# Kernel tuning notes

Measured on AMD Instinct MI355X. Metric: run time of the kernel, lower is better.

## Reference

```python
import jax, jax.numpy as jnp
import numpy as np

B, C, H, W = 64, 1, 128, 128
R = 4               # regiao_tamanho
GH, GW = H // R, W // R
N = GH * GW         # out_neurons = 1024
D, S = 16, 32       # n_dendritos, n_sinapses


def setup_inputs() -> dict:
    key = jax.random.key(0)
    kx, kw = jax.random.split(key)
    x = jax.random.normal(kx, (B, C, H, W), dtype=jnp.float32)
    pesos = jax.random.normal(kw, (N, D, S, R, R), dtype=jnp.float32)
    return {"x": x, "pesos": pesos}


def reference(x, pesos):
    # x: [B, 1, H, W] -> non-overlapping RxR patches: [B, 1, GH, R, GW, R]
    xp = x.reshape(B, C, GH, R, GW, R)
    # torch.einsum('bcrr,...') with repeated 'r' takes the PATCH DIAGONAL
    # (and sums over c). xd[b, i, j, r] = sum_c x[b, c, i*R+r, j*R+r]
    xd = jnp.einsum('bcirjr->bijr', xp).reshape(B, N, R)   # [B, N, R]
    # weight diagonal: wd[n, d, s, r] = pesos[n, d, s, r, r]
    wd = jnp.einsum('ndsrr->ndsr', pesos)                  # [N, D, S, R]
    # per-region unshared contraction over the diagonal index r
    out = jnp.einsum('bnr,ndsr->bnds', xd, wd)             # [B, N, D, S]
    return out
```

## Files before the change

kernel.cpp:

```cpp
#include <hip/hip_runtime.h>

#define B 64
#define H 128
#define W 128
#define R 4
#define GW 32
#define N 1024
#define D 16
#define S 32

typedef float vf4 __attribute__((ext_vector_type(4)));

__global__ __launch_bounds__(128) void conexao_regional_kernel(
    const float* __restrict__ x,
    const float* __restrict__ pesos,
    float* __restrict__ out)
{
    __shared__ float sx[B][R];

    const int n   = blockIdx.x;
    const int tid = threadIdx.x;

    const int i = n / GW, j = n % GW;
    const int xbase = i * (R * W) + j * R;
    for (int t = tid; t < B * R; t += 128) {
        const int b = t >> 2, r = t & 3;
        sx[b][r] = x[b * (H * W) + xbase + r * (W + 1)];
    }
    __syncthreads();

    const int  e0    = tid * 4;
    const long pbase = ((long)n * 512 + e0) * 16;
    float w[4][4];
#pragma unroll
    for (int k = 0; k < 4; ++k) {
        const vf4* p = (const vf4*)(pesos + pbase + (long)k * 16);
        const vf4 q0 = __builtin_nontemporal_load(p + 0);
        const vf4 q1 = __builtin_nontemporal_load(p + 1);
        const vf4 q2 = __builtin_nontemporal_load(p + 2);
        const vf4 q3 = __builtin_nontemporal_load(p + 3);
        w[k][0] = q0.x;
        w[k][1] = q1.y;
        w[k][2] = q2.z;
        w[k][3] = q3.w;
    }

    float* outp = out + (long)n * 512 + e0;
#pragma unroll 8
    for (int b = 0; b < B; ++b) {
        const vf4 xv = *(const vf4*)&sx[b][0];
        vf4 v;
        v.x = w[0][0] * xv.x + w[0][1] * xv.y + w[0][2] * xv.z + w[0][3] * xv.w;
        v.y = w[1][0] * xv.x + w[1][1] * xv.y + w[1][2] * xv.z + w[1][3] * xv.w;
        v.z = w[2][0] * xv.x + w[2][1] * xv.y + w[2][2] * xv.z + w[2][3] * xv.w;
        v.w = w[3][0] * xv.x + w[3][1] * xv.y + w[3][2] * xv.z + w[3][3] * xv.w;
        __builtin_nontemporal_store(v, (vf4*)(outp + (long)b * (N * D * S)));
    }
}

extern "C" void kernel_launch(void* const* d_in, const int* in_sizes, int n_in,
                              void* d_out, int out_size, void* d_ws, size_t ws_size,
                              hipStream_t stream) {
    const float* x     = (const float*)d_in[0];
    const float* pesos = (const float*)d_in[1];
    float* out = (float*)d_out;

    conexao_regional_kernel<<<N, 128, 0, stream>>>(x, pesos, out);
}
```

Measured before the change: 177.2 us.

## Split batch across four blocks per region and drop nontemporal hints

```diff
diff --git a/kernel.cpp b/kernel.cpp
--- a/kernel.cpp
+++ b/kernel.cpp
@@ -9,25 +9,31 @@
 #define D 16
 #define S 32
 
+
+#define BSPLIT 4
+#define BPB (B / BSPLIT)
+
 typedef float vf4 __attribute__((ext_vector_type(4)));
 
-__global__ __launch_bounds__(128) void conexao_regional_kernel(
+__global__ __launch_bounds__(128, 8) void conexao_regional_kernel(
     const float* __restrict__ x,
     const float* __restrict__ pesos,
     float* __restrict__ out)
 {
-    __shared__ float sx[B][R];
+    __shared__ float sx[BPB][R];
 
-    const int n   = blockIdx.x;
-    const int tid = threadIdx.x;
+    const int blk   = blockIdx.x;
+    const int chunk = blk >> 10;
+    const int n     = blk & (N - 1);
+    const int tid   = threadIdx.x;
+    const int b0    = chunk * BPB;
 
     const int i = n / GW, j = n % GW;
     const int xbase = i * (R * W) + j * R;
-    for (int t = tid; t < B * R; t += 128) {
-        const int b = t >> 2, r = t & 3;
-        sx[b][r] = x[b * (H * W) + xbase + r * (W + 1)];
+    if (tid < BPB * R) {
+        const int b = tid >> 2, r = tid & 3;
+        sx[b][r] = x[(b0 + b) * (H * W) + xbase + r * (W + 1)];
     }
-    __syncthreads();
 
     const int  e0    = tid * 4;
     const long pbase = ((long)n * 512 + e0) * 16;
@@ -35,26 +41,27 @@
 #pragma unroll
     for (int k = 0; k < 4; ++k) {
         const vf4* p = (const vf4*)(pesos + pbase + (long)k * 16);
-        const vf4 q0 = __builtin_nontemporal_load(p + 0);
-        const vf4 q1 = __builtin_nontemporal_load(p + 1);
-        const vf4 q2 = __builtin_nontemporal_load(p + 2);
-        const vf4 q3 = __builtin_nontemporal_load(p + 3);
+        const vf4 q0 = p[0];
+        const vf4 q1 = p[1];
+        const vf4 q2 = p[2];
+        const vf4 q3 = p[3];
         w[k][0] = q0.x;
         w[k][1] = q1.y;
         w[k][2] = q2.z;
         w[k][3] = q3.w;
     }
+    __syncthreads();
 
-    float* outp = out + (long)n * 512 + e0;
-#pragma unroll 8
-    for (int b = 0; b < B; ++b) {
-        const vf4 xv = *(const vf4*)&sx[b][0];
+    float* outp = out + (long)b0 * (N * D * S) + (long)n * 512 + e0;
+#pragma unroll
+    for (int bb = 0; bb < BPB; ++bb) {
+        const vf4 xv = *(const vf4*)&sx[bb][0];
         vf4 v;
         v.x = w[0][0] * xv.x + w[0][1] * xv.y + w[0][2] * xv.z + w[0][3] * xv.w;
         v.y = w[1][0] * xv.x + w[1][1] * xv.y + w[1][2] * xv.z + w[1][3] * xv.w;
         v.z = w[2][0] * xv.x + w[2][1] * xv.y + w[2][2] * xv.z + w[2][3] * xv.w;
         v.w = w[3][0] * xv.x + w[3][1] * xv.y + w[3][2] * xv.z + w[3][3] * xv.w;
-        __builtin_nontemporal_store(v, (vf4*)(outp + (long)b * (N * D * S)));
+        *(vf4*)(outp + (long)bb * (N * D * S)) = v;
     }
 }
 
@@ -65,5 +72,5 @@
     const float* pesos = (const float*)d_in[1];
     float* out = (float*)d_out;
 
-    conexao_regional_kernel<<<N, 128, 0, stream>>>(x, pesos, out);
+    conexao_regional_kernel<<<N * BSPLIT, 128, 0, stream>>>(x, pesos, out);
 }
```

Result: no change. 176.9 us (-0.2%).
